# Performance work log

Measured on AMD Instinct MI355X. Metric: run time of the kernel, lower is better.

The kernel has to match this reference:

```python
import jax, jax.numpy as jnp
import numpy as np

B, S, E = 512, 200, 128
H, D = 4, 32  # att_head_nums, singlehead_emb_size; H*D == E (required by residual)
FF = 4 * H * D


def setup_inputs() -> dict:
    key = jax.random.key(0)
    ks = jax.random.split(key, 12)
    sc = 0.02
    return {
        "queries": jax.random.normal(ks[0], (B, S, E), jnp.float32),
        "keys": jax.random.normal(ks[1], (B, S, E), jnp.float32),
        "keys_mask": jax.random.randint(ks[2], (B, S), 0, 2) > 0,
        "Wq": jax.random.normal(ks[3], (H * D, E), jnp.float32) * sc,
        "bq": jnp.zeros((H * D,), jnp.float32),
        "Wk": jax.random.normal(ks[4], (H * D, E), jnp.float32) * sc,
        "bk": jnp.zeros((H * D,), jnp.float32),
        "Wv": jax.random.normal(ks[5], (H * D, E), jnp.float32) * sc,
        "bv": jnp.zeros((H * D,), jnp.float32),
        "W1": jax.random.normal(ks[6], (FF, H * D), jnp.float32) * sc,
        "b1": jnp.zeros((FF,), jnp.float32),
        "W2": jax.random.normal(ks[7], (H * D, FF), jnp.float32) * sc,
        "b2": jnp.zeros((H * D,), jnp.float32),
    }


def reference(queries, keys, keys_mask, Wq, bq, Wk, bk, Wv, bv, W1, b1, W2, b2):
    # QKV projections (nn.Linear: x @ W.T + b)
    Q = queries @ Wq.T + bq                         # [B,S,H*D]
    K = keys @ Wk.T + bk
    V = keys @ Wv.T + bv
    Qh = Q.reshape(B, S, H, D).transpose(0, 2, 1, 3)  # [B,H,S,D]
    Kh = K.reshape(B, S, H, D).transpose(0, 2, 1, 3)
    Vh = V.reshape(B, S, H, D).transpose(0, 2, 1, 3)
    scores = jnp.einsum('bhqd,bhkd->bhqk', Qh, Kh) / jnp.sqrt(jnp.float32(D))
    scores = jnp.where(keys_mask[:, None, None, :], scores, -jnp.inf)
    probs = jax.nn.softmax(scores, axis=-1)
    out = jnp.einsum('bhqk,bhkd->bhqd', probs, Vh)   # [B,H,S,D]
    out = out.transpose(0, 2, 1, 3).reshape(B, S, H * D)
    out = out + queries                              # residual (use_res=True)
    # FFN with residual (use_feed_forward=True, no layer norm, dropout=0)
    ff = jax.nn.relu(out @ W1.T + b1) @ W2.T + b2
    return ff + out
```

## Files before the change

kernel.cpp:

```cpp
#include <hip/hip_runtime.h>

#define B_  512
#define S_  200
#define M_  102400

typedef short bf16x8 __attribute__((ext_vector_type(8)));
typedef float f32x4  __attribute__((ext_vector_type(4)));
typedef unsigned short u16;
typedef u16 us4 __attribute__((ext_vector_type(4)));
typedef unsigned int u32;

#define MFMA16 __builtin_amdgcn_mfma_f32_16x16x32_bf16
#define GLDS(gp, lp) __builtin_amdgcn_global_load_lds( \
    (const __attribute__((address_space(1))) unsigned int*)(gp), \
    (__attribute__((address_space(3))) unsigned int*)(lp), 16, 0, 0)

__device__ __forceinline__ u16 f2bf(float f) {
    union { float f; unsigned u; } v; v.f = f;
    unsigned r = v.u + 0x7fffu + ((v.u >> 16) & 1u);
    return (u16)(r >> 16);
}
__device__ __forceinline__ float bf2f(u16 x) {
    union { unsigned u; float f; } v; v.u = ((unsigned)x) << 16;
    return v.f;
}
__device__ __forceinline__ u32 pk(float a, float b) {
    return (__float_as_uint(a) >> 16) | (__float_as_uint(b) & 0xffff0000u);
}
__device__ __forceinline__ int swz(int row, int b) { return b ^ ((row & 7) << 4); }

#define WQ_OFF   0
#define WK_OFF   16384
#define WV_OFF   32768
#define W1_OFF   49152
#define W2_OFF   114688
#define BQS_OFF  180224
#define QB_OFF   262144
#define KB_OFF   (QB_OFF + 13107200)
#define VB_OFF   (KB_OFF + 13107200)

__global__ __launch_bounds__(256) void cvt_kernel(
    const float* __restrict__ Wq, const float* __restrict__ bq,
    const float* __restrict__ Wk, const float* __restrict__ Wv,
    const float* __restrict__ W1, const float* __restrict__ W2,
    u16* __restrict__ wdst, float* __restrict__ bqs)
{
    const float QSC = 0.17677669529663689f * 1.4426950408889634f;
    int idx = blockIdx.x * 256 + threadIdx.x;
    if (idx < 128) bqs[idx] = bq[idx] * QSC;
    if (idx < 49152) {
        int wsel = idx >> 14, r = (idx >> 7) & 127, c = idx & 127;
        const float* src = wsel == 0 ? Wq : (wsel == 1 ? Wk : Wv);
        float v = src[idx & 16383];
        if (wsel == 0) v *= QSC;
        *(u16*)((char*)(wdst + wsel * 16384) + r * 256 + swz(r, 2 * c)) = f2bf(v);
    } else if (idx < 114688) {
        int i = idx - 49152;
        int r_g = i >> 7, c = i & 127;
        int sub = r_g >> 6, fr = r_g & 63;
        *(u16*)((char*)(wdst + W1_OFF) + sub * 16384 + fr * 256 + ((2 * c) ^ ((fr & 7) << 4)))
            = f2bf(W1[i]);
    } else if (idx < 180224) {
        int i = idx - 114688;
        int r_out = i >> 9, c_ff = i & 511;
        int sub = c_ff >> 6, o = c_ff & 63;
        int chunk = o >> 5, w32 = o & 31;
        int bb = w32 >> 4, hh = (w32 >> 2) & 3, rr = w32 & 3;
        int lc = chunk * 32 + 8 * hh + 4 * bb + rr;
        *(u16*)((char*)(wdst + W2_OFF) + sub * 16384 + r_out * 128 + ((2 * lc) ^ ((r_out & 7) << 4)))
            = f2bf(W2[i]);
    }
}

__global__ __launch_bounds__(256) void proj_q_kernel(
    const float* __restrict__ X, const u16* __restrict__ Ws,
    const float* __restrict__ bqs, u16* __restrict__ Y)
{
    __shared__ __align__(16) u16 sW[16384];
    const int tid = threadIdx.x, w = tid >> 6, lane = tid & 63;
    const int lo = lane & 15, hi = lane >> 4;
    const int base = blockIdx.x * 128;

#pragma unroll
    for (int k = 0; k < 8; ++k) {
        int seg = w * 8 + k;
        GLDS((const char*)Ws + seg * 1024 + lane * 16, (char*)sW + seg * 1024);
    }

    bf16x8 a[2][4];
#pragma unroll
    for (int t = 0; t < 2; ++t) {
        const float* rp = X + (size_t)(base + w * 32 + t * 16 + lo) * 128;
#pragma unroll
        for (int ks = 0; ks < 4; ++ks) {
            float4 v0 = *(const float4*)(rp + ks * 32 + hi * 8);
            float4 v1 = *(const float4*)(rp + ks * 32 + hi * 8 + 4);
            union { bf16x8 v; u16 s[8]; } af;
            af.s[0]=f2bf(v0.x); af.s[1]=f2bf(v0.y); af.s[2]=f2bf(v0.z); af.s[3]=f2bf(v0.w);
            af.s[4]=f2bf(v1.x); af.s[5]=f2bf(v1.y); af.s[6]=f2bf(v1.z); af.s[7]=f2bf(v1.w);
            a[t][ks] = af.v;
        }
    }
    asm volatile("s_waitcnt vmcnt(0)" ::: "memory");
    __builtin_amdgcn_s_barrier();

#pragma unroll
    for (int n = 0; n < 8; ++n) {
        bf16x8 bf[4];
#pragma unroll
        for (int ks = 0; ks < 4; ++ks)
            bf[ks] = *(const bf16x8*)((const char*)sW + (n*16+lo)*256 + swz(lo, ks*64 + hi*16));
        float bb = bqs[n * 16 + lo];
#pragma unroll
        for (int t = 0; t < 2; ++t) {
            f32x4 acc = {0.f, 0.f, 0.f, 0.f};
#pragma unroll
            for (int ks = 0; ks < 4; ++ks) acc = MFMA16(a[t][ks], bf[ks], acc, 0, 0, 0);
#pragma unroll
            for (int r = 0; r < 4; ++r) {
                int row = base + w * 32 + t * 16 + hi * 4 + r;
                *(u16*)((char*)Y + (size_t)row * 256 + swz(row, n * 32 + 2 * lo)) =
                    f2bf(acc[r] + bb);
            }
        }
    }
}

__global__ __launch_bounds__(256) void proj_kv_kernel(
    const float* __restrict__ X, const u16* __restrict__ Wks, const u16* __restrict__ Wvs,
    const float* __restrict__ bk, const float* __restrict__ bv,
    u16* __restrict__ K, u16* __restrict__ V)
{
    __shared__ __align__(16) u16 sWk[16384];
    __shared__ __align__(16) u16 sWv[16384];
    const int tid = threadIdx.x, w = tid >> 6, lane = tid & 63;
    const int lo = lane & 15, hi = lane >> 4;
    const int base = blockIdx.x * 128;

#pragma unroll
    for (int k = 0; k < 8; ++k) {
        int seg = w * 8 + k;
        GLDS((const char*)Wks + seg * 1024 + lane * 16, (char*)sWk + seg * 1024);
        GLDS((const char*)Wvs + seg * 1024 + lane * 16, (char*)sWv + seg * 1024);
    }

    bf16x8 a[2][4];
#pragma unroll
    for (int t = 0; t < 2; ++t) {
        const float* rp = X + (size_t)(base + w * 32 + t * 16 + lo) * 128;
#pragma unroll
        for (int ks = 0; ks < 4; ++ks) {
            float4 v0 = *(const float4*)(rp + ks * 32 + hi * 8);
            float4 v1 = *(const float4*)(rp + ks * 32 + hi * 8 + 4);
            union { bf16x8 v; u16 s[8]; } af;
            af.s[0]=f2bf(v0.x); af.s[1]=f2bf(v0.y); af.s[2]=f2bf(v0.z); af.s[3]=f2bf(v0.w);
            af.s[4]=f2bf(v1.x); af.s[5]=f2bf(v1.y); af.s[6]=f2bf(v1.z); af.s[7]=f2bf(v1.w);
            a[t][ks] = af.v;
        }
    }
    asm volatile("s_waitcnt vmcnt(0)" ::: "memory");
    __builtin_amdgcn_s_barrier();

#pragma unroll
    for (int n = 0; n < 8; ++n) {
        bf16x8 bf[4];
#pragma unroll
        for (int ks = 0; ks < 4; ++ks)
            bf[ks] = *(const bf16x8*)((const char*)sWk + (n*16+lo)*256 + swz(lo, ks*64 + hi*16));
        float bb = bk[n * 16 + lo];
#pragma unroll
        for (int t = 0; t < 2; ++t) {
            f32x4 acc = {0.f, 0.f, 0.f, 0.f};
#pragma unroll
            for (int ks = 0; ks < 4; ++ks) acc = MFMA16(a[t][ks], bf[ks], acc, 0, 0, 0);
#pragma unroll
            for (int r = 0; r < 4; ++r) {
                size_t row = base + w * 32 + t * 16 + hi * 4 + r;
                K[row * 128 + n * 16 + lo] = f2bf(acc[r] + bb);
            }
        }
    }
#pragma unroll
    for (int n = 0; n < 8; ++n) {
        bf16x8 bf[4];
#pragma unroll
        for (int ks = 0; ks < 4; ++ks)
            bf[ks] = *(const bf16x8*)((const char*)sWv + (n*16+lo)*256 + swz(lo, ks*64 + hi*16));
        float bb = bv[n * 16 + lo];
#pragma unroll
        for (int t = 0; t < 2; ++t) {
            f32x4 acc = {0.f, 0.f, 0.f, 0.f};
#pragma unroll
            for (int ks = 0; ks < 4; ++ks) acc = MFMA16(a[t][ks], bf[ks], acc, 0, 0, 0);
#pragma unroll
            for (int r = 0; r < 4; ++r) {
                size_t row = base + w * 32 + t * 16 + hi * 4 + r;
                V[row * 128 + n * 16 + lo] = f2bf(acc[r] + bb);
            }
        }
    }
}

__global__ __launch_bounds__(256, 5) void attn_kernel(
    const u16* __restrict__ Qb, const u16* __restrict__ Kb, const u16* __restrict__ Vb,
    const int* __restrict__ mask, const float* __restrict__ queries, u16* __restrict__ Xb)
{
    __shared__ __align__(16) u16 sK[200][40];
    __shared__ __align__(16) u16 sVt[32][248];
    __shared__ __align__(16) u16 sMk[224];

    const int bid = blockIdx.x;
    const int wg  = (bid & 7) * 256 + (bid >> 3);
    const int b   = wg >> 2;
    const int h   = wg & 3;
    const int tid = threadIdx.x;
    const size_t rowbase = (size_t)b * 200;

    for (int slot = tid; slot < 800; slot += 256) {
        int s = slot >> 2, part = slot & 3;
        *(bf16x8*)&sK[s][part * 8] =
            *(const bf16x8*)(Kb + (rowbase + s) * 128 + h * 32 + part * 8);
    }
    for (int slot = tid; slot < 1792; slot += 256) {
        int d = slot & 31, sg = slot >> 5;
        int s0 = sg * 4;
        int c0 = s0 & ~31, a = (s0 & 31) >> 2;
        int pos = c0 + (a & 3) * 8 + (a >> 2) * 4;
        us4 v;
#pragma unroll
        for (int j = 0; j < 4; ++j) {
            int s = s0 + j;
            bool ok = (s < 200) && (mask[rowbase + s] != 0);
            v[j] = ok ? Vb[(rowbase + s) * 128 + h * 32 + d] : (u16)0;
        }
        *(us4*)&sVt[d][pos] = v;
    }
    for (int i = tid; i < 224; i += 256) {
        int c0 = i & ~31, local = i & 31;
        int hh = local >> 3, j = local & 7;
        int key = c0 + 16 * (j >> 2) + 4 * hh + (j & 3);
        sMk[i] = (key < 200 && mask[rowbase + key] != 0) ? (u16)0x3F80 : (u16)0;
    }
    __syncthreads();

    const int w = tid >> 6, lane = tid & 63;
    const int lo = lane & 15, hi = lane >> 4;

    for (int qb = w; qb < 13; qb += 4) {
        int qrow = qb * 16 + lo;
        if (qrow > 199) qrow = 199;
        bf16x8 qf = *(const bf16x8*)((const char*)Qb + (size_t)(rowbase + qrow) * 256
                                      + swz(qrow, h * 64 + hi * 16));

        f32x4 acc0 = {0.f, 0.f, 0.f, 0.f};
        f32x4 acc1 = {0.f, 0.f, 0.f, 0.f};
        f32x4 accs = {0.f, 0.f, 0.f, 0.f};

        auto chunk = [&](int c0, bf16x8 k0, bf16x8 k1) {
            f32x4 z = {0.f, 0.f, 0.f, 0.f};
            f32x4 s0 = MFMA16(k0, qf, z, 0, 0, 0);
            f32x4 s1 = MFMA16(k1, qf, z, 0, 0, 0);
            float p0, p1, p2, p3, p4, p5, p6, p7;
            asm("v_exp_f32 %0, %1" : "=v"(p0) : "v"(s0[0]));
            asm("v_exp_f32 %0, %1" : "=v"(p1) : "v"(s0[1]));
            asm("v_exp_f32 %0, %1" : "=v"(p2) : "v"(s0[2]));
            asm("v_exp_f32 %0, %1" : "=v"(p3) : "v"(s0[3]));
            asm("v_exp_f32 %0, %1" : "=v"(p4) : "v"(s1[0]));
            asm("v_exp_f32 %0, %1" : "=v"(p5) : "v"(s1[1]));
            asm("v_exp_f32 %0, %1" : "=v"(p6) : "v"(s1[2]));
            asm("v_exp_f32 %0, %1" : "=v"(p7) : "v"(s1[3]));
            union { bf16x8 v; u32 d[4]; } pa;
            asm("v_cvt_pk_bf16_f32 %0, %1, %2" : "=v"(pa.d[0]) : "v"(p0), "v"(p1));
            asm("v_cvt_pk_bf16_f32 %0, %1, %2" : "=v"(pa.d[1]) : "v"(p2), "v"(p3));
            asm("v_cvt_pk_bf16_f32 %0, %1, %2" : "=v"(pa.d[2]) : "v"(p4), "v"(p5));
            asm("v_cvt_pk_bf16_f32 %0, %1, %2" : "=v"(pa.d[3]) : "v"(p6), "v"(p7));
            bf16x8 mkf = *(const bf16x8*)&sMk[c0 + hi * 8];
            bf16x8 v0  = *(const bf16x8*)&sVt[lo][c0 + hi * 8];
            bf16x8 v1  = *(const bf16x8*)&sVt[16 + lo][c0 + hi * 8];
            acc0 = MFMA16(pa.v, v0, acc0, 0, 0, 0);
            acc1 = MFMA16(pa.v, v1, acc1, 0, 0, 0);
            accs = MFMA16(pa.v, mkf, accs, 0, 0, 0);
        };

#pragma unroll 1
        for (int kt = 0; kt < 6; ++kt) {
            int c0 = kt * 32;
            bf16x8 k0 = *(const bf16x8*)&sK[c0 + lo][hi * 8];
            bf16x8 k1 = *(const bf16x8*)&sK[c0 + 16 + lo][hi * 8];
            chunk(c0, k0, k1);
        }
        {
            int r0 = 192 + lo; if (r0 > 199) r0 = 199;
            bf16x8 k0 = *(const bf16x8*)&sK[r0][hi * 8];
            bf16x8 k1 = *(const bf16x8*)&sK[199][hi * 8];
            chunk(192, k0, k1);
        }

        float invr[4];
#pragma unroll
        for (int r = 0; r < 4; ++r) invr[r] = __builtin_amdgcn_rcpf(accs[r]);
#pragma unroll
        for (int r = 0; r < 4; ++r) {
            int row = qb * 16 + hi * 4 + r;
            if (row < 200) {
                size_t o  = (rowbase + row) * 128 + h * 32;
                size_t rb = (rowbase + row) * 256;
                *(u16*)((char*)Xb + rb + swz(row, h * 64 + 2 * lo)) =
                    f2bf(acc0[r] * invr[r] + queries[o + lo]);
                *(u16*)((char*)Xb + rb + swz(row, h * 64 + 32 + 2 * lo)) =
                    f2bf(acc1[r] * invr[r] + queries[o + 16 + lo]);
            }
        }
    }
}

__global__ __launch_bounds__(256, 2) void ffn_kernel(
    const u16* __restrict__ Xb, const u16* __restrict__ W1s, const u16* __restrict__ W2s,
    const float* __restrict__ b1, const float* __restrict__ b2, float* __restrict__ out)
{
    __shared__ __align__(16) u16 sW1[2][8192];
    __shared__ __align__(16) u16 sW2[2][8192];
    const int tid = threadIdx.x, w = tid >> 6, lane = tid & 63;
    const int lo = lane & 15, hi = lane >> 4;
    const size_t base = (size_t)blockIdx.x * 128;
    const int wrow = w * 32;

#pragma unroll
    for (int k = 0; k < 4; ++k) {
        int seg = w * 4 + k;
        GLDS((const char*)W1s + seg * 1024 + lane * 16, (char*)sW1[0] + seg * 1024);
        GLDS((const char*)W2s + seg * 1024 + lane * 16, (char*)sW2[0] + seg * 1024);
    }

    bf16x8 a[2][4];
#pragma unroll
    for (int t = 0; t < 2; ++t) {
        size_t row = base + wrow + t * 16 + lo;
#pragma unroll
        for (int ks = 0; ks < 4; ++ks)
            a[t][ks] = *(const bf16x8*)((const char*)Xb + row * 256
                                         + ((ks * 64 + hi * 16) ^ ((lo & 7) << 4)));
    }

    f32x4 yacc[2][8];
#pragma unroll
    for (int t = 0; t < 2; ++t)
#pragma unroll
        for (int n = 0; n < 8; ++n) yacc[t][n] = (f32x4){0.f, 0.f, 0.f, 0.f};

    asm volatile("s_waitcnt vmcnt(0)" ::: "memory");
    __builtin_amdgcn_s_barrier();

    for (int sub = 0; sub < 8; ++sub) {
        int cur = sub & 1, nxt = cur ^ 1;
        if (sub < 7) {
#pragma unroll
            for (int k = 0; k < 4; ++k) {
                int seg = w * 4 + k;
                GLDS((const char*)W1s + (sub + 1) * 16384 + seg * 1024 + lane * 16,
                     (char*)sW1[nxt] + seg * 1024);
                GLDS((const char*)W2s + (sub + 1) * 16384 + seg * 1024 + lane * 16,
                     (char*)sW2[nxt] + seg * 1024);
            }
        }
#pragma unroll
        for (int c = 0; c < 2; ++c) {
            bf16x8 w1f[2][4];
#pragma unroll
            for (int u = 0; u < 2; ++u)
#pragma unroll
                for (int ks = 0; ks < 4; ++ks)
                    w1f[u][ks] = *(const bf16x8*)((const char*)sW1[cur]
                                   + ((2*c+u) * 16 + lo) * 256
                                   + ((ks * 64 + hi * 16) ^ ((lo & 7) << 4)));
            float4 b1v0 = *(const float4*)(b1 + sub * 64 + (2*c) * 16 + 4 * hi);
            float4 b1v1 = *(const float4*)(b1 + sub * 64 + (2*c+1) * 16 + 4 * hi);
            bf16x8 pb[2];
#pragma unroll
            for (int t = 0; t < 2; ++t) {
                f32x4 h0 = {0.f,0.f,0.f,0.f}, h1 = {0.f,0.f,0.f,0.f};
#pragma unroll
                for (int ks = 0; ks < 4; ++ks) {
                    h0 = MFMA16(w1f[0][ks], a[t][ks], h0, 0, 0, 0);
                    h1 = MFMA16(w1f[1][ks], a[t][ks], h1, 0, 0, 0);
                }
                float p0 = fmaxf(h0[0] + b1v0.x, 0.f);
                float p1 = fmaxf(h0[1] + b1v0.y, 0.f);
                float p2 = fmaxf(h0[2] + b1v0.z, 0.f);
                float p3 = fmaxf(h0[3] + b1v0.w, 0.f);
                float p4 = fmaxf(h1[0] + b1v1.x, 0.f);
                float p5 = fmaxf(h1[1] + b1v1.y, 0.f);
                float p6 = fmaxf(h1[2] + b1v1.z, 0.f);
                float p7 = fmaxf(h1[3] + b1v1.w, 0.f);
                union { bf16x8 v; u32 d[4]; } pu;
                pu.d[0] = pk(p0, p1); pu.d[1] = pk(p2, p3);
                pu.d[2] = pk(p4, p5); pu.d[3] = pk(p6, p7);
                pb[t] = pu.v;
            }
#pragma unroll
            for (int n = 0; n < 8; ++n) {
                bf16x8 w2f = *(const bf16x8*)((const char*)sW2[cur]
                               + (n * 16 + lo) * 128
                               + ((c * 64 + hi * 16) ^ ((lo & 7) << 4)));
                yacc[0][n] = MFMA16(w2f, pb[0], yacc[0][n], 0, 0, 0);
                yacc[1][n] = MFMA16(w2f, pb[1], yacc[1][n], 0, 0, 0);
            }
        }
        asm volatile("s_waitcnt vmcnt(0)" ::: "memory");
        __builtin_amdgcn_s_barrier();
    }

#pragma unroll
    for (int t = 0; t < 2; ++t) {
        size_t row = base + wrow + t * 16 + lo;
#pragma unroll
        for (int n = 0; n < 8; ++n) {
            float4 b2v = *(const float4*)(b2 + n * 16 + 4 * hi);
            us4 rv = *(const us4*)((const char*)Xb + row * 256
                                    + ((2 * (n * 16 + 4 * hi)) ^ (((int)row & 7) << 4)));
            float4 o;
            o.x = yacc[t][n][0] + b2v.x + bf2f(rv[0]);
            o.y = yacc[t][n][1] + b2v.y + bf2f(rv[1]);
            o.z = yacc[t][n][2] + b2v.z + bf2f(rv[2]);
            o.w = yacc[t][n][3] + b2v.w + bf2f(rv[3]);
            *(float4*)(out + row * 128 + n * 16 + 4 * hi) = o;
        }
    }
}

extern "C" void kernel_launch(void* const* d_in, const int* in_sizes, int n_in,
                              void* d_out, int out_size, void* d_ws, size_t ws_size,
                              hipStream_t stream) {
    const float* queries = (const float*)d_in[0];
    const float* keys    = (const float*)d_in[1];
    const int*   mask    = (const int*)d_in[2];
    const float* Wq = (const float*)d_in[3];
    const float* bq = (const float*)d_in[4];
    const float* Wk = (const float*)d_in[5];
    const float* bk = (const float*)d_in[6];
    const float* Wv = (const float*)d_in[7];
    const float* bv = (const float*)d_in[8];
    const float* W1 = (const float*)d_in[9];
    const float* b1 = (const float*)d_in[10];
    const float* W2 = (const float*)d_in[11];
    const float* b2 = (const float*)d_in[12];
    float* out = (float*)d_out;

    u16* wbase = (u16*)d_ws;
    u16* Qb = wbase + QB_OFF;
    u16* Kb = wbase + KB_OFF;
    u16* Vb = wbase + VB_OFF;
    float* bqs = (float*)(wbase + BQS_OFF);

    cvt_kernel<<<704, 256, 0, stream>>>(Wq, bq, Wk, Wv, W1, W2, wbase, bqs);
    proj_q_kernel<<<800, 256, 0, stream>>>(queries, wbase + WQ_OFF, bqs, Qb);
    proj_kv_kernel<<<800, 256, 0, stream>>>(keys, wbase + WK_OFF, wbase + WV_OFF,
                                            bk, bv, Kb, Vb);
    attn_kernel<<<B_ * 4, 256, 0, stream>>>(Qb, Kb, Vb, mask, queries, Qb);
    ffn_kernel<<<800, 256, 0, stream>>>(Qb, wbase + W1_OFF, wbase + W2_OFF, b1, b2, out);
}
```

Before: 148.8 us.

## Compact unmasked keys per batch to skip masked key chunks in attention

The attention kernel now ballots the key mask, builds a compacted index list of valid keys in shared memory, and gathers only those K/V rows. The key loop then runs over only the padded count of valid keys instead of a fixed 7 chunks. With a random mask about half the keys are masked, so this cuts QK/PV MFMA work and K/V loads roughly in half. In exchange it adds a ballot, an extra barrier and indirect gathers, and the launch-bounds occupancy hint drops from 5 to 4. It also swaps inline-asm exp and convert instructions for builtins and a pk helper.

Result: faster. 127.9 us (-14.1%).

```diff
diff --git a/kernel.cpp b/kernel.cpp
--- a/kernel.cpp
+++ b/kernel.cpp
@@ -201,50 +201,68 @@
     }
 }
 
-__global__ __launch_bounds__(256, 5) void attn_kernel(
+__global__ __launch_bounds__(256, 4) void attn_kernel(
     const u16* __restrict__ Qb, const u16* __restrict__ Kb, const u16* __restrict__ Vb,
     const int* __restrict__ mask, const float* __restrict__ queries, u16* __restrict__ Xb)
 {
-    __shared__ __align__(16) u16 sK[200][40];
+    __shared__ __align__(16) u16 sK[224][40];
     __shared__ __align__(16) u16 sVt[32][248];
     __shared__ __align__(16) u16 sMk[224];
+    __shared__ u16 sIdx[224];
+    __shared__ int sCnt4[4];
 
     const int bid = blockIdx.x;
     const int wg  = (bid & 7) * 256 + (bid >> 3);
     const int b   = wg >> 2;
     const int h   = wg & 3;
     const int tid = threadIdx.x;
+    const int w = tid >> 6, lane = tid & 63;
+    const int lo = lane & 15, hi = lane >> 4;
     const size_t rowbase = (size_t)b * 200;
 
-    for (int slot = tid; slot < 800; slot += 256) {
-        int s = slot >> 2, part = slot & 3;
-        *(bf16x8*)&sK[s][part * 8] =
-            *(const bf16x8*)(Kb + (rowbase + s) * 128 + h * 32 + part * 8);
-    }
-    for (int slot = tid; slot < 1792; slot += 256) {
+    bool valid = (tid < 200) && (mask[rowbase + tid] != 0);
+    unsigned long long bal = __ballot(valid);
+    int prefix = __popcll(bal & ((1ull << lane) - 1ull));
+    if (lane == 0) sCnt4[w] = __popcll(bal);
+    __syncthreads();
+
+    int c0_ = sCnt4[0], c1_ = sCnt4[1], c2_ = sCnt4[2], c3_ = sCnt4[3];
+    int off = (w > 0 ? c0_ : 0) + (w > 1 ? c1_ : 0) + (w > 2 ? c2_ : 0);
+    const int cnt = c0_ + c1_ + c2_ + c3_;
+    const int cntPad = (cnt + 31) & ~31;
+    const int nch = cntPad >> 5;
+    if (valid) sIdx[off + prefix] = (u16)tid;
+    for (int i = tid; i < 224; i += 256) {
+        int cb = i & ~31, local = i & 31;
+        int hh = local >> 3, j = local & 7;
+        int slot = cb + 16 * (j >> 2) + 4 * hh + (j & 3);
+        sMk[i] = (slot < cnt) ? (u16)0x3F80 : (u16)0;
+    }
+    __syncthreads();
+
+    for (int i = tid; i < (cntPad << 2); i += 256) {
+        int j = i >> 2, part = i & 3;
+        bf16x8 val = {0,0,0,0,0,0,0,0};
+        if (j < cnt) {
+            int key = sIdx[j];
+            val = *(const bf16x8*)(Kb + (rowbase + key) * 128 + h * 32 + part * 8);
+        }
+        *(bf16x8*)&sK[j][part * 8] = val;
+    }
+    for (int slot = tid; slot < (cntPad << 3); slot += 256) {
         int d = slot & 31, sg = slot >> 5;
         int s0 = sg * 4;
-        int c0 = s0 & ~31, a = (s0 & 31) >> 2;
-        int pos = c0 + (a & 3) * 8 + (a >> 2) * 4;
+        int cb = s0 & ~31, a = (s0 & 31) >> 2;
+        int pos = cb + (a & 3) * 8 + (a >> 2) * 4;
         us4 v;
 #pragma unroll
         for (int j = 0; j < 4; ++j) {
             int s = s0 + j;
-            bool ok = (s < 200) && (mask[rowbase + s] != 0);
-            v[j] = ok ? Vb[(rowbase + s) * 128 + h * 32 + d] : (u16)0;
+            v[j] = (s < cnt) ? Vb[(rowbase + sIdx[s]) * 128 + h * 32 + d] : (u16)0;
         }
         *(us4*)&sVt[d][pos] = v;
     }
-    for (int i = tid; i < 224; i += 256) {
-        int c0 = i & ~31, local = i & 31;
-        int hh = local >> 3, j = local & 7;
-        int key = c0 + 16 * (j >> 2) + 4 * hh + (j & 3);
-        sMk[i] = (key < 200 && mask[rowbase + key] != 0) ? (u16)0x3F80 : (u16)0;
-    }
     __syncthreads();
-
-    const int w = tid >> 6, lane = tid & 63;
-    const int lo = lane & 15, hi = lane >> 4;
 
     for (int qb = w; qb < 13; qb += 4) {
         int qrow = qb * 16 + lo;
@@ -256,44 +274,31 @@
         f32x4 acc1 = {0.f, 0.f, 0.f, 0.f};
         f32x4 accs = {0.f, 0.f, 0.f, 0.f};
 
-        auto chunk = [&](int c0, bf16x8 k0, bf16x8 k1) {
+#pragma unroll 1
+        for (int kt = 0; kt < nch; ++kt) {
+            int cb = kt * 32;
+            bf16x8 k0 = *(const bf16x8*)&sK[cb + lo][hi * 8];
+            bf16x8 k1 = *(const bf16x8*)&sK[cb + 16 + lo][hi * 8];
             f32x4 z = {0.f, 0.f, 0.f, 0.f};
             f32x4 s0 = MFMA16(k0, qf, z, 0, 0, 0);
             f32x4 s1 = MFMA16(k1, qf, z, 0, 0, 0);
-            float p0, p1, p2, p3, p4, p5, p6, p7;
-            asm("v_exp_f32 %0, %1" : "=v"(p0) : "v"(s0[0]));
-            asm("v_exp_f32 %0, %1" : "=v"(p1) : "v"(s0[1]));
-            asm("v_exp_f32 %0, %1" : "=v"(p2) : "v"(s0[2]));
-            asm("v_exp_f32 %0, %1" : "=v"(p3) : "v"(s0[3]));
-            asm("v_exp_f32 %0, %1" : "=v"(p4) : "v"(s1[0]));
-            asm("v_exp_f32 %0, %1" : "=v"(p5) : "v"(s1[1]));
-            asm("v_exp_f32 %0, %1" : "=v"(p6) : "v"(s1[2]));
-            asm("v_exp_f32 %0, %1" : "=v"(p7) : "v"(s1[3]));
+            float p0 = __builtin_amdgcn_exp2f(s0[0]);
+            float p1 = __builtin_amdgcn_exp2f(s0[1]);
+            float p2 = __builtin_amdgcn_exp2f(s0[2]);
+            float p3 = __builtin_amdgcn_exp2f(s0[3]);
+            float p4 = __builtin_amdgcn_exp2f(s1[0]);
+            float p5 = __builtin_amdgcn_exp2f(s1[1]);
+            float p6 = __builtin_amdgcn_exp2f(s1[2]);
+            float p7 = __builtin_amdgcn_exp2f(s1[3]);
             union { bf16x8 v; u32 d[4]; } pa;
-            asm("v_cvt_pk_bf16_f32 %0, %1, %2" : "=v"(pa.d[0]) : "v"(p0), "v"(p1));
-            asm("v_cvt_pk_bf16_f32 %0, %1, %2" : "=v"(pa.d[1]) : "v"(p2), "v"(p3));
-            asm("v_cvt_pk_bf16_f32 %0, %1, %2" : "=v"(pa.d[2]) : "v"(p4), "v"(p5));
-            asm("v_cvt_pk_bf16_f32 %0, %1, %2" : "=v"(pa.d[3]) : "v"(p6), "v"(p7));
-            bf16x8 mkf = *(const bf16x8*)&sMk[c0 + hi * 8];
-            bf16x8 v0  = *(const bf16x8*)&sVt[lo][c0 + hi * 8];
-            bf16x8 v1  = *(const bf16x8*)&sVt[16 + lo][c0 + hi * 8];
+            pa.d[0] = pk(p0, p1); pa.d[1] = pk(p2, p3);
+            pa.d[2] = pk(p4, p5); pa.d[3] = pk(p6, p7);
+            bf16x8 mkf = *(const bf16x8*)&sMk[cb + hi * 8];
+            bf16x8 v0  = *(const bf16x8*)&sVt[lo][cb + hi * 8];
+            bf16x8 v1  = *(const bf16x8*)&sVt[16 + lo][cb + hi * 8];
             acc0 = MFMA16(pa.v, v0, acc0, 0, 0, 0);
             acc1 = MFMA16(pa.v, v1, acc1, 0, 0, 0);
             accs = MFMA16(pa.v, mkf, accs, 0, 0, 0);
-        };
-
-#pragma unroll 1
-        for (int kt = 0; kt < 6; ++kt) {
-            int c0 = kt * 32;
-            bf16x8 k0 = *(const bf16x8*)&sK[c0 + lo][hi * 8];
-            bf16x8 k1 = *(const bf16x8*)&sK[c0 + 16 + lo][hi * 8];
-            chunk(c0, k0, k1);
-        }
-        {
-            int r0 = 192 + lo; if (r0 > 199) r0 = 199;
-            bf16x8 k0 = *(const bf16x8*)&sK[r0][hi * 8];
-            bf16x8 k1 = *(const bf16x8*)&sK[199][hi * 8];
-            chunk(192, k0, k1);
         }
 
         float invr[4];
```
